# Kernel tuning notes

Hardware: AMD Instinct MI355X
Metric: run time of the kernel (lower is better)

Reference implementation:

```python
import jax, jax.numpy as jnp
import numpy as np

D_IN, H, H1, H2 = 50, 64, 32, 1

def setup_inputs() -> dict:
    key = jax.random.key(0)
    ks = jax.random.split(key, 13)
    s = 1.0 / np.sqrt(H)
    u = lambda k, shp: jax.random.uniform(k, shp, jnp.float32, -s, s)
    x = jax.random.normal(ks[0], (512, 2048, D_IN), jnp.float32)
    return {
        "x": x,
        "W_ih0": u(ks[1], (H, D_IN)), "W_hh0": u(ks[2], (H, H)),
        "b_ih0": u(ks[3], (H,)),      "b_hh0": u(ks[4], (H,)),
        "W_ih1": u(ks[5], (H, H)),    "W_hh1": u(ks[6], (H, H)),
        "b_ih1": u(ks[7], (H,)),      "b_hh1": u(ks[8], (H,)),
        "W1": u(ks[9], (H1, H)),      "b1": u(ks[10], (H1,)),
        "W2": u(ks[11], (H2, H1)),    "b2": u(ks[12], (H2,)),
    }

def reference(x, W_ih0, W_hh0, b_ih0, b_hh0, W_ih1, W_hh1, b_ih1, b_hh1, W1, b1, W2, b2):
    B = x.shape[0]
    # Precompute input projections for layer 0 for all timesteps: [S, B, H]
    xt = jnp.swapaxes(x, 0, 1)  # [S, B, D_IN]
    x_proj0 = jnp.einsum('sbd,hd->sbh', xt, W_ih0) + b_ih0 + b_hh0

    h0 = jnp.zeros((B, H), x.dtype)

    def step(carry, xp):
        h1, h2 = carry
        h1 = jnp.tanh(xp + h1 @ W_hh0.T)
        h2 = jnp.tanh(h1 @ W_ih1.T + b_ih1 + h2 @ W_hh1.T + b_hh1)
        return (h1, h2), None

    (h1f, h2f), _ = jax.lax.scan(step, (h0, h0), x_proj0)
    hidden = jax.nn.relu(h2f @ W1.T + b1)
    return jax.nn.sigmoid(hidden @ W2.T + b2)
```

## Files before the change

kernel.cpp:

```cpp
#include <hip/hip_runtime.h>

#define S_LEN 2048
#define DIN   50
#define H     64
#define XB    32
#define XPROWS (XB + 1)
#define XRPAD  52
#define XRAWN  (XPROWS * XRPAD)

__device__ __forceinline__ float tanh_fast(float v) {
    float e = __builtin_amdgcn_exp2f(v * 2.885390082f);
    return 1.0f - 2.0f * __builtin_amdgcn_rcpf(e + 1.0f);
}

__device__ __forceinline__ float red4(float v) {
#if __has_builtin(__builtin_amdgcn_permlane16_swap) && __has_builtin(__builtin_amdgcn_permlane32_swap)
    typedef unsigned u2 __attribute__((ext_vector_type(2)));
    u2 r = __builtin_amdgcn_permlane16_swap(__float_as_uint(v), __float_as_uint(v), false, false);
    float s = __uint_as_float(r[0]) + __uint_as_float(r[1]);
    u2 q = __builtin_amdgcn_permlane32_swap(__float_as_uint(s), __float_as_uint(s), false, false);
    return __uint_as_float(q[0]) + __uint_as_float(q[1]);
#else
    v += __shfl_xor(v, 16, 64);
    v += __shfl_xor(v, 32, 64);
    return v;
#endif
}

__global__ __launch_bounds__(256)
__attribute__((amdgpu_waves_per_eu(2, 2)))
void rnn_fused(const float* __restrict__ x,
               const float* __restrict__ W_ih0, const float* __restrict__ W_hh0,
               const float* __restrict__ b_ih0, const float* __restrict__ b_hh0,
               const float* __restrict__ W_ih1, const float* __restrict__ W_hh1,
               const float* __restrict__ b_ih1, const float* __restrict__ b_hh1,
               const float* __restrict__ W1, const float* __restrict__ b1,
               const float* __restrict__ W2, const float* __restrict__ b2,
               float* __restrict__ out)
{
    const int b    = blockIdx.x;
    const int tid  = threadIdx.x;
    const int lane = tid & 63;
    const int w    = tid >> 6;
    const int j    = lane & 15;
    const int kg   = lane >> 4;
    const int outj = 16 * w + j;

    __shared__ __align__(16) float xraw[XRAWN];
    __shared__ __align__(16) float xp[XPROWS][H];
    __shared__ __align__(16) float h1s[2][H];
    __shared__ __align__(16) float h2s[2][H];

    float wxf[DIN];
    #pragma unroll
    for (int d = 0; d < DIN; ++d) wxf[d] = W_ih0[lane * DIN + d];
    const float bias0 = b_ih0[lane] + b_hh0[lane];

    float whh0_l[16], wih1_l[16], whh1_l[16];
    #pragma unroll
    for (int i = 0; i < 16; ++i) {
        whh0_l[i] = W_hh0[outj * H + 16 * kg + i];
        wih1_l[i] = W_ih1[outj * H + 16 * kg + i];
        whh1_l[i] = W_hh1[outj * H + 16 * kg + i];
    }
    const float bias1 = b_ih1[outj] + b_hh1[outj];

    const float* __restrict__ xrow = x + (size_t)b * (size_t)(S_LEN * DIN);

    auto refill = [&](int T) {
        #pragma unroll
        for (int r = 0; r < 7; ++r) {
            int f = tid + 256 * r;
            if (f < XRAWN) {
                int row = f / XRPAD;
                int col = f - row * XRPAD;
                int t   = T + row;
                float v = 0.0f;
                if (col < DIN && t < S_LEN) v = xrow[(size_t)t * DIN + col];
                xraw[f] = v;
            }
        }
        __syncthreads();
        #pragma unroll
        for (int r = 0; r < 9; ++r) {
            int u = w + 4 * r;
            if (u < XPROWS) {
                const float4* xr4 = (const float4*)&xraw[u * XRPAD];
                float a0 = bias0, a1 = 0.0f;
                #pragma unroll
                for (int q = 0; q < 12; ++q) {
                    float4 v = xr4[q];
                    a0 = fmaf(v.x, wxf[4 * q + 0], a0);
                    a1 = fmaf(v.y, wxf[4 * q + 1], a1);
                    a0 = fmaf(v.z, wxf[4 * q + 2], a0);
                    a1 = fmaf(v.w, wxf[4 * q + 3], a1);
                }
                float2 vt = *(const float2*)&xraw[u * XRPAD + 48];
                a0 = fmaf(vt.x, wxf[48], a0);
                a1 = fmaf(vt.y, wxf[49], a1);
                xp[u][lane] = a0 + a1;
            }
        }
        __syncthreads();
    };

    float h1c[16], h2c[16];
    const float* xpp0 = &xp[0][outj];

    refill(0);
    {
        float h1n = tanh_fast(xpp0[0]);
        if (kg == 0) h1s[0][outj] = h1n;
        if (tid < 64) h2s[1][lane] = 0.0f;
    }
    __syncthreads();

#define INTERVAL(PAR, NPAR, XPIDX)                                             \
    {                                                                          \
        *(float4*)&h1c[0]  = *(const float4*)&h1s[PAR][16 * kg + 0];           \
        *(float4*)&h1c[4]  = *(const float4*)&h1s[PAR][16 * kg + 4];           \
        *(float4*)&h1c[8]  = *(const float4*)&h1s[PAR][16 * kg + 8];           \
        *(float4*)&h1c[12] = *(const float4*)&h1s[PAR][16 * kg + 12];          \
        *(float4*)&h2c[0]  = *(const float4*)&h2s[NPAR][16 * kg + 0];          \
        *(float4*)&h2c[4]  = *(const float4*)&h2s[NPAR][16 * kg + 4];          \
        *(float4*)&h2c[8]  = *(const float4*)&h2s[NPAR][16 * kg + 8];          \
        *(float4*)&h2c[12] = *(const float4*)&h2s[NPAR][16 * kg + 12];         \
        float xpn = xpp0[(XPIDX) * H];                                         \
                 \
        float c0 = 0, c1 = 0, c2 = 0, c3 = 0;                                  \
        _Pragma("unroll")                                                      \
        for (int q = 0; q < 4; ++q) {                                          \
            c0 = fmaf(h1c[4 * q + 0], wih1_l[4 * q + 0], c0);                  \
            c1 = fmaf(h1c[4 * q + 1], wih1_l[4 * q + 1], c1);                  \
            c2 = fmaf(h1c[4 * q + 2], wih1_l[4 * q + 2], c2);                  \
            c3 = fmaf(h1c[4 * q + 3], wih1_l[4 * q + 3], c3);                  \
        }                                                                      \
        _Pragma("unroll")                                                      \
        for (int q = 0; q < 4; ++q) {                                          \
            c0 = fmaf(h2c[4 * q + 0], whh1_l[4 * q + 0], c0);                  \
            c1 = fmaf(h2c[4 * q + 1], whh1_l[4 * q + 1], c1);                  \
            c2 = fmaf(h2c[4 * q + 2], whh1_l[4 * q + 2], c2);                  \
            c3 = fmaf(h2c[4 * q + 3], whh1_l[4 * q + 3], c3);                  \
        }                                                                      \
        float h2n = tanh_fast(red4((c0 + c1) + (c2 + c3)) + bias1);            \
                            \
        float a0 = 0, a1 = 0, a2 = 0, a3 = 0;                                  \
        _Pragma("unroll")                                                      \
        for (int q = 0; q < 4; ++q) {                                          \
            a0 = fmaf(h1c[4 * q + 0], whh0_l[4 * q + 0], a0);                  \
            a1 = fmaf(h1c[4 * q + 1], whh0_l[4 * q + 1], a1);                  \
            a2 = fmaf(h1c[4 * q + 2], whh0_l[4 * q + 2], a2);                  \
            a3 = fmaf(h1c[4 * q + 3], whh0_l[4 * q + 3], a3);                  \
        }                                                                      \
        float h1n = tanh_fast(red4((a0 + a1) + (a2 + a3)) + xpn);              \
        if (kg == 0) {                                                         \
            h2s[PAR][outj]  = h2n;                                             \
            h1s[NPAR][outj] = h1n;                                             \
        }                                                                      \
        __syncthreads();                                                       \
    }

    for (int T = 0; T < S_LEN; T += XB) {
        if (T) refill(T);
        #pragma unroll
        for (int ui = 0; ui < XB; ui += 2) {
            INTERVAL(0, 1, ui + 1)
            INTERVAL(1, 0, ui + 2)
        }
    }
#undef INTERVAL

    if (tid < 64) {
        float hv = 0.0f;
        if (lane < 32) {
            float acc = b1[lane];
            #pragma unroll
            for (int k = 0; k < H; ++k)
                acc = fmaf(h2s[1][k], W1[lane * H + k], acc);
            hv = fmaxf(acc, 0.0f) * W2[lane];
        }
        #pragma unroll
        for (int off = 32; off; off >>= 1)
            hv += __shfl_xor(hv, off, 64);
        if (lane == 0)
            out[b] = 1.0f / (1.0f + __expf(-(hv + b2[0])));
    }
}

extern "C" void kernel_launch(void* const* d_in, const int* in_sizes, int n_in,
                              void* d_out, int out_size, void* d_ws, size_t ws_size,
                              hipStream_t stream) {
    const float* x     = (const float*)d_in[0];
    const float* W_ih0 = (const float*)d_in[1];
    const float* W_hh0 = (const float*)d_in[2];
    const float* b_ih0 = (const float*)d_in[3];
    const float* b_hh0 = (const float*)d_in[4];
    const float* W_ih1 = (const float*)d_in[5];
    const float* W_hh1 = (const float*)d_in[6];
    const float* b_ih1 = (const float*)d_in[7];
    const float* b_hh1 = (const float*)d_in[8];
    const float* W1    = (const float*)d_in[9];
    const float* b1    = (const float*)d_in[10];
    const float* W2    = (const float*)d_in[11];
    const float* b2    = (const float*)d_in[12];
    float* out = (float*)d_out;

    rnn_fused<<<dim3(512), dim3(256), 0, stream>>>(
        x, W_ih0, W_hh0, b_ih0, b_hh0,
        W_ih1, W_hh1, b_ih1, b_hh1,
        W1, b1, W2, b2, out);
}
```

Before: 993.0 us.

## Split layer-0 input projection across waves by input-column chunks

The x-projection refill now splits the 50 input columns into four 13-column chunks, one per wave, instead of giving each wave whole timestep rows with all 50 weights. Each wave writes a partial sum into a 4-slot shared buffer, and the recurrence reads a float4 and sums it. This cuts per-thread weight registers from 50 to 13, which may help occupancy or register pressure, and spreads the projection work evenly across waves. In exchange there is more shared-memory traffic, a lane-rotated slot index to spread bank use, and an extra reduction on the serial recurrence path.

```diff
diff --git a/kernel.cpp b/kernel.cpp
--- a/kernel.cpp
+++ b/kernel.cpp
@@ -5,8 +5,6 @@
 #define H     64
 #define XB    32
 #define XPROWS (XB + 1)
-#define XRPAD  52
-#define XRAWN  (XPROWS * XRPAD)
 
 __device__ __forceinline__ float tanh_fast(float v) {
     float e = __builtin_amdgcn_exp2f(v * 2.885390082f);
@@ -46,14 +44,17 @@
     const int kg   = lane >> 4;
     const int outj = 16 * w + j;
 
-    __shared__ __align__(16) float xraw[XRAWN];
-    __shared__ __align__(16) float xp[XPROWS][H];
+    __shared__ __align__(16) float xraw[XPROWS][4][16];
+    __shared__ __align__(16) float xp4[XPROWS][H][4];
     __shared__ __align__(16) float h1s[2][H];
     __shared__ __align__(16) float h2s[2][H];
 
-    float wxf[DIN];
+    float wxc[13];
     #pragma unroll
-    for (int d = 0; d < DIN; ++d) wxf[d] = W_ih0[lane * DIN + d];
+    for (int i = 0; i < 13; ++i) {
+        int c = 13 * w + i;
+        wxc[i] = (c < DIN) ? W_ih0[lane * DIN + c] : 0.0f;
+    }
     const float bias0 = b_ih0[lane] + b_hh0[lane];
 
     float whh0_l[16], wih1_l[16], whh1_l[16];
@@ -67,49 +68,48 @@
 
     const float* __restrict__ xrow = x + (size_t)b * (size_t)(S_LEN * DIN);
 
+    const int xslot = (w + (lane >> 2)) & 3;
+
     auto refill = [&](int T) {
         #pragma unroll
         for (int r = 0; r < 7; ++r) {
             int f = tid + 256 * r;
-            if (f < XRAWN) {
-                int row = f / XRPAD;
-                int col = f - row * XRPAD;
-                int t   = T + row;
+            if (f < XPROWS * 52) {
+                int u   = f / 52;
+                int rem = f - u * 52;
+                int c   = rem / 13;
+                int jj  = rem - 13 * c;
+                int col = 13 * c + jj;
+                int t   = T + u;
                 float v = 0.0f;
                 if (col < DIN && t < S_LEN) v = xrow[(size_t)t * DIN + col];
-                xraw[f] = v;
+                xraw[u][c][jj] = v;
             }
         }
         __syncthreads();
-        #pragma unroll
-        for (int r = 0; r < 9; ++r) {
-            int u = w + 4 * r;
-            if (u < XPROWS) {
-                const float4* xr4 = (const float4*)&xraw[u * XRPAD];
-                float a0 = bias0, a1 = 0.0f;
-                #pragma unroll
-                for (int q = 0; q < 12; ++q) {
-                    float4 v = xr4[q];
-                    a0 = fmaf(v.x, wxf[4 * q + 0], a0);
-                    a1 = fmaf(v.y, wxf[4 * q + 1], a1);
-                    a0 = fmaf(v.z, wxf[4 * q + 2], a0);
-                    a1 = fmaf(v.w, wxf[4 * q + 3], a1);
-                }
-                float2 vt = *(const float2*)&xraw[u * XRPAD + 48];
-                a0 = fmaf(vt.x, wxf[48], a0);
-                a1 = fmaf(vt.y, wxf[49], a1);
-                xp[u][lane] = a0 + a1;
-            }
+        for (int u = 0; u < XPROWS; ++u) {
+            const float4* xr = (const float4*)&xraw[u][w][0];
+            float4 A = xr[0], B = xr[1], C = xr[2];
+            float  d = xraw[u][w][12];
+            float a0 = (w == 0) ? bias0 : 0.0f, a1 = 0.0f;
+            a0 = fmaf(A.x, wxc[0],  a0);  a1 = fmaf(A.y, wxc[1],  a1);
+            a0 = fmaf(A.z, wxc[2],  a0);  a1 = fmaf(A.w, wxc[3],  a1);
+            a0 = fmaf(B.x, wxc[4],  a0);  a1 = fmaf(B.y, wxc[5],  a1);
+            a0 = fmaf(B.z, wxc[6],  a0);  a1 = fmaf(B.w, wxc[7],  a1);
+            a0 = fmaf(C.x, wxc[8],  a0);  a1 = fmaf(C.y, wxc[9],  a1);
+            a0 = fmaf(C.z, wxc[10], a0);  a1 = fmaf(C.w, wxc[11], a1);
+            a0 = fmaf(d,   wxc[12], a0);
+            xp4[u][lane][xslot] = a0 + a1;
         }
         __syncthreads();
     };
 
     float h1c[16], h2c[16];
-    const float* xpp0 = &xp[0][outj];
 
     refill(0);
     {
-        float h1n = tanh_fast(xpp0[0]);
+        float4 p4 = *(const float4*)&xp4[0][outj][0];
+        float h1n = tanh_fast((p4.x + p4.y) + (p4.z + p4.w));
         if (kg == 0) h1s[0][outj] = h1n;
         if (tid < 64) h2s[1][lane] = 0.0f;
     }
@@ -125,7 +125,8 @@
         *(float4*)&h2c[4]  = *(const float4*)&h2s[NPAR][16 * kg + 4];          \
         *(float4*)&h2c[8]  = *(const float4*)&h2s[NPAR][16 * kg + 8];          \
         *(float4*)&h2c[12] = *(const float4*)&h2s[NPAR][16 * kg + 12];         \
-        float xpn = xpp0[(XPIDX) * H];                                         \
+        float4 p4 = *(const float4*)&xp4[XPIDX][outj][0];                      \
+        float xpn = (p4.x + p4.y) + (p4.z + p4.w);                             \
                  \
         float c0 = 0, c1 = 0, c2 = 0, c3 = 0;                                  \
         _Pragma("unroll")                                                      \
```

Result: slower. 1.085 ms (+9.2%).
